# Kernel optimization log

Hardware: AMD Instinct MI355X
Metric: run time of the kernel (lower is better)

## Reference

```python
import jax, jax.numpy as jnp
import numpy as np

B, C, L, D, E, K = 64, 23, 26000, 64, 512, 3  # batch, chromosomes, bins/chr, d_model, eos_dim, num_states
V = C * L


def setup_inputs() -> dict:
    key = jax.random.key(0)
    k0, k1, k2, k3 = jax.random.split(key, 4)
    return {
        "eos_emb": jax.random.normal(k0, (B, C, E), jnp.float32),
        "bin_ids": jnp.arange(C * L, dtype=jnp.int32).reshape(C, L),
        "emb_table": jax.random.normal(k1, (V, D), jnp.float32) * 0.02,
        "eos_W": jax.random.normal(k2, (D, E), jnp.float32) / np.float32(np.sqrt(E)),
        "eos_b": jnp.zeros((D,), jnp.float32),
        "fc_W": jax.random.normal(k3, (K, 2 * D), jnp.float32) / np.float32(np.sqrt(2 * D)),
        "fc_b": jnp.zeros((K,), jnp.float32),
    }


def reference(eos_emb, bin_ids, emb_table, eos_W, eos_b, fc_W, fc_b):
    # eos_projection (use_eos_proj=True): [B,C,E] @ [D,E]^T + b -> [B,C,D]
    eos = jnp.einsum('bce,de->bcd', eos_emb, eos_W) + eos_b
    # per-chromosome embedding gather (bin_projection skipped: bin_emb_dim == d_model, use_bin_proj=False)
    bin_emb = emb_table[bin_ids]  # [C,L,D]
    # fc on concat([bin, eos]) == bin @ Wb^T + eos @ We^T + b (avoids materializing [B,C,L,2D])
    Wb, We = fc_W[:, :D], fc_W[:, D:]
    a = jnp.einsum('cld,kd->clk', bin_emb, Wb)          # [C,L,K]
    e = jnp.einsum('bcd,kd->bck', eos, We) + fc_b       # [B,C,K]
    return jax.nn.relu(a[None, :, :, :] + e[:, :, None, :])  # [B,C,L,K]
```

## Files before the change

kernel.cpp:

```cpp
#include <hip/hip_runtime.h>

#define NB 64
#define NC 23
#define NL 26000
#define ND 64
#define NE 512
#define NK 3
#define FP4   (NL * NK / 4)
#define CFP4  (NC * FP4)
#define CHUNK 438
#define NCHUNK 1024
#define GLSPAN 584

typedef float v4f __attribute__((ext_vector_type(4)));

__global__ __launch_bounds__(256) void eos_e_kernel(
    const float* __restrict__ eos_emb,
    const float* __restrict__ eos_W,
    const float* __restrict__ eos_b,
    const float* __restrict__ fc_W,
    const float* __restrict__ fc_b,
    float* __restrict__ e_out)
{
    const int bc = blockIdx.x;
    const int t  = threadIdx.x;
    const int q  = t & 3;
    const int d  = t >> 2;

    __shared__ v4f xs4[NE / 4];
    if (t < NE / 4)
        xs4[t] = reinterpret_cast<const v4f*>(eos_emb + (size_t)bc * NE)[t];
    __syncthreads();

    const v4f* wrow = reinterpret_cast<const v4f*>(eos_W + (size_t)d * NE);
    v4f acc = (v4f)(0.f);
    #pragma unroll 8
    for (int j = 0; j < NE / 16; ++j) {
        const int idx = q + 4 * j;
        acc += wrow[idx] * xs4[idx];
    }
    float p = (acc.x + acc.y) + (acc.z + acc.w);
    p += __shfl_xor(p, 1, 64);
    p += __shfl_xor(p, 2, 64);
    const float eosd = p + eos_b[d];

    __shared__ float part[4][NK];
    #pragma unroll
    for (int k = 0; k < NK; ++k) {
        float pk = eosd * fc_W[k * (2 * ND) + ND + d];
        pk += __shfl_xor(pk,  4, 64);
        pk += __shfl_xor(pk,  8, 64);
        pk += __shfl_xor(pk, 16, 64);
        pk += __shfl_xor(pk, 32, 64);
        if ((t & 63) == 0) part[t >> 6][k] = pk;
    }
    __syncthreads();
    if (t < NK)
        e_out[(size_t)bc * NK + t] =
            part[0][t] + part[1][t] + part[2][t] + part[3][t] + fc_b[t];
}

__global__ __launch_bounds__(256) void fused_kernel(
    const int*   __restrict__ bin_ids,
    const float* __restrict__ emb_table,
    const float* __restrict__ fc_W,
    const float* __restrict__ e_in,
    float* __restrict__ out)
{
    const int bx    = blockIdx.x;
    const int t     = threadIdx.x;
    const int base  = bx * CHUNK;
    const int gl_lo = bx * GLSPAN;

    __shared__ v4f   wb4[NK][ND / 4];
    __shared__ v4f   e4[3][NB][2];
    __shared__ float a_lds[GLSPAN * 3];

    const int c_lo = base / FP4;
    const int c_hi_raw = (base + CHUNK - 1) / FP4;
    const int c_hi = (c_hi_raw < NC) ? c_hi_raw : (NC - 1);

    if (t < NK * (ND / 4)) {
        const int k = t / (ND / 4), i = t % (ND / 4);
        wb4[k][i] = reinterpret_cast<const v4f*>(fc_W + (size_t)k * (2 * ND))[i];
    }
    {
        const int i = t;
        for (int it = i; it < 3 * NB * 2; it += 256) {
            const int p   = it / (NB * 2);
            const int rem = it - p * (NB * 2);
            const int bl  = rem >> 1;
            const int ci  = rem & 1;
            const int c   = ci ? c_hi : c_lo;
            const float* ep = e_in + ((size_t)bl * NC + c) * NK;
            const float e0 = ep[0], e1 = ep[1], e2 = ep[2];
            v4f v;
            if      (p == 0) { v.x = e0; v.y = e1; v.z = e2; v.w = e0; }
            else if (p == 1) { v.x = e1; v.y = e2; v.z = e0; v.w = e1; }
            else             { v.x = e2; v.y = e0; v.z = e1; v.w = e2; }
            e4[p][bl][ci] = v;
        }
    }
    __syncthreads();

    const int q = t & 3;
    const int r = t >> 2;
    #pragma unroll
    for (int pass = 0; pass < 10; ++pass) {
        const int rl = pass * 64 + r;
        const int gl = gl_lo + rl;
        if (rl < GLSPAN && gl < NC * NL) {
            const int row = bin_ids[gl];
            const v4f* er = reinterpret_cast<const v4f*>(emb_table + (size_t)row * ND);
            v4f s0 = (v4f)(0.f), s1 = (v4f)(0.f), s2 = (v4f)(0.f);
            #pragma unroll
            for (int j = 0; j < 4; ++j) {
                const int idx = q + 4 * j;
                const v4f v = er[idx];
                s0 += v * wb4[0][idx];
                s1 += v * wb4[1][idx];
                s2 += v * wb4[2][idx];
            }
            float a0 = (s0.x + s0.y) + (s0.z + s0.w);
            float a1 = (s1.x + s1.y) + (s1.z + s1.w);
            float a2 = (s2.x + s2.y) + (s2.z + s2.w);
            a0 += __shfl_xor(a0, 1, 64); a0 += __shfl_xor(a0, 2, 64);
            a1 += __shfl_xor(a1, 1, 64); a1 += __shfl_xor(a1, 2, 64);
            a2 += __shfl_xor(a2, 1, 64); a2 += __shfl_xor(a2, 2, 64);
            if (q < NK) {
                const float val = (q == 0) ? a0 : (q == 1) ? a1 : a2;
                a_lds[rl * 3 + q] = val;
            }
        }
    }
    __syncthreads();

    const int f0 = base + t;
    const int p0 = f0 % 3;
    const int ci0 = ((f0 / FP4) == c_lo) ? 0 : 1;
    const bool v0 = (f0 < CFP4);
    v4f a0v = (v4f)(0.f);
    if (v0) a0v = *reinterpret_cast<const v4f*>(&a_lds[t * 4]);

    const int t1 = 256 + t;
    const bool has1 = (t1 < CHUNK);
    const int f1 = base + t1;
    const int p1 = has1 ? (f1 % 3) : 0;
    const int ci1 = (has1 && (f1 / FP4) == c_lo) ? 0 : 1;
    const bool v1 = has1 && (f1 < CFP4);
    v4f a1v = (v4f)(0.f);
    if (v1) a1v = *reinterpret_cast<const v4f*>(&a_lds[t1 * 4]);

    v4f* o4 = reinterpret_cast<v4f*>(out);
    #pragma unroll 4
    for (int bl = 0; bl < NB; ++bl) {
        const size_t ob = (size_t)bl * CFP4;
        if (v0) {
            const v4f ev = e4[p0][bl][ci0];
            v4f o;
            o.x = fmaxf(a0v.x + ev.x, 0.f);
            o.y = fmaxf(a0v.y + ev.y, 0.f);
            o.z = fmaxf(a0v.z + ev.z, 0.f);
            o.w = fmaxf(a0v.w + ev.w, 0.f);
            __builtin_nontemporal_store(o, &o4[ob + f0]);
        }
        if (v1) {
            const v4f ev = e4[p1][bl][ci1];
            v4f o;
            o.x = fmaxf(a1v.x + ev.x, 0.f);
            o.y = fmaxf(a1v.y + ev.y, 0.f);
            o.z = fmaxf(a1v.z + ev.z, 0.f);
            o.w = fmaxf(a1v.w + ev.w, 0.f);
            __builtin_nontemporal_store(o, &o4[ob + f1]);
        }
    }
}

__global__ __launch_bounds__(256) void decoder_fused_kernel(
    const int*   __restrict__ bin_ids,
    const float* __restrict__ emb_table,
    const float* __restrict__ fc_W,
    const float* __restrict__ e_in,
    float* __restrict__ out)
{
    const int c   = blockIdx.y;
    const int tid = threadIdx.x;
    const int l   = blockIdx.x * 256 + tid;

    __shared__ float wb[NK][ND];
    __shared__ float es[NB * NK];

    if (tid < NK * ND)
        wb[tid / ND][tid % ND] = fc_W[(tid / ND) * (2 * ND) + (tid % ND)];
    if (tid < NB * NK) {
        int b = tid / NK, k = tid % NK;
        es[tid] = e_in[((size_t)b * NC + c) * NK + k];
    }
    __syncthreads();
    if (l >= NL) return;

    const int row = bin_ids[(size_t)c * NL + l];
    const float4* er = reinterpret_cast<const float4*>(emb_table + (size_t)row * ND);
    const float4* w0 = reinterpret_cast<const float4*>(wb[0]);
    const float4* w1 = reinterpret_cast<const float4*>(wb[1]);
    const float4* w2 = reinterpret_cast<const float4*>(wb[2]);

    float a0 = 0.f, a1 = 0.f, a2 = 0.f;
    #pragma unroll
    for (int i = 0; i < ND / 4; ++i) {
        float4 v  = er[i];
        float4 p0 = w0[i], p1 = w1[i], p2 = w2[i];
        a0 += v.x * p0.x + v.y * p0.y + v.z * p0.z + v.w * p0.w;
        a1 += v.x * p1.x + v.y * p1.y + v.z * p1.z + v.w * p1.w;
        a2 += v.x * p2.x + v.y * p2.y + v.z * p2.z + v.w * p2.w;
    }

    size_t obase = ((size_t)c * NL + l) * NK;
    const size_t bstride = (size_t)NC * NL * NK;
    #pragma unroll 4
    for (int b = 0; b < NB; ++b) {
        const float e0 = es[b * NK + 0];
        const float e1 = es[b * NK + 1];
        const float e2 = es[b * NK + 2];
        out[obase + 0] = fmaxf(a0 + e0, 0.f);
        out[obase + 1] = fmaxf(a1 + e1, 0.f);
        out[obase + 2] = fmaxf(a2 + e2, 0.f);
        obase += bstride;
    }
}

extern "C" void kernel_launch(void* const* d_in, const int* in_sizes, int n_in,
                              void* d_out, int out_size, void* d_ws, size_t ws_size,
                              hipStream_t stream) {
    const float* eos_emb   = (const float*)d_in[0];
    const int*   bin_ids   = (const int*)  d_in[1];
    const float* emb_table = (const float*)d_in[2];
    const float* eos_W     = (const float*)d_in[3];
    const float* eos_b     = (const float*)d_in[4];
    const float* fc_W      = (const float*)d_in[5];
    const float* fc_b      = (const float*)d_in[6];
    float*       out       = (float*)d_out;

    float* e_ws = (float*)d_ws;

    eos_e_kernel<<<NB * NC, 256, 0, stream>>>(eos_emb, eos_W, eos_b, fc_W, fc_b, e_ws);

    if (ws_size >= (size_t)NB * NC * NK * sizeof(float)) {
        fused_kernel<<<NCHUNK, 256, 0, stream>>>(bin_ids, emb_table, fc_W, e_ws, out);
    } else {
        dim3 grid((NL + 255) / 256, NC);
        decoder_fused_kernel<<<grid, 256, 0, stream>>>(bin_ids, emb_table, fc_W, e_ws, out);
    }
}
```

Baseline: 153.3 us.

## Merge eos projection and decoder into one cooperative kernel with grid sync

```diff
diff --git a/kernel.cpp b/kernel.cpp
--- a/kernel.cpp
+++ b/kernel.cpp
@@ -1,4 +1,6 @@
 #include <hip/hip_runtime.h>
+#include <hip/hip_cooperative_groups.h>
+namespace cg = cooperative_groups;
 
 #define NB 64
 #define NC 23
@@ -8,102 +10,93 @@
 #define NK 3
 #define FP4   (NL * NK / 4)
 #define CFP4  (NC * FP4)
+#define NBLK  1024
 #define CHUNK 438
-#define NCHUNK 1024
 #define GLSPAN 584
+#define NBC (NB * NC)
 
 typedef float v4f __attribute__((ext_vector_type(4)));
 
-__global__ __launch_bounds__(256) void eos_e_kernel(
+__global__ __launch_bounds__(256, 4) void coop_kernel(
     const float* __restrict__ eos_emb,
+    const int*   __restrict__ bin_ids,
+    const float* __restrict__ emb_table,
     const float* __restrict__ eos_W,
     const float* __restrict__ eos_b,
     const float* __restrict__ fc_W,
     const float* __restrict__ fc_b,
-    float* __restrict__ e_out)
+    float* __restrict__ e_ws,
+    float* __restrict__ out)
 {
-    const int bc = blockIdx.x;
+    const int bx = blockIdx.x;
     const int t  = threadIdx.x;
     const int q  = t & 3;
     const int d  = t >> 2;
 
-    __shared__ v4f xs4[NE / 4];
-    if (t < NE / 4)
-        xs4[t] = reinterpret_cast<const v4f*>(eos_emb + (size_t)bc * NE)[t];
-    __syncthreads();
-
-    const v4f* wrow = reinterpret_cast<const v4f*>(eos_W + (size_t)d * NE);
-    v4f acc = (v4f)(0.f);
-    #pragma unroll 8
-    for (int j = 0; j < NE / 16; ++j) {
-        const int idx = q + 4 * j;
-        acc += wrow[idx] * xs4[idx];
-    }
-    float p = (acc.x + acc.y) + (acc.z + acc.w);
-    p += __shfl_xor(p, 1, 64);
-    p += __shfl_xor(p, 2, 64);
-    const float eosd = p + eos_b[d];
-
+    __shared__ v4f   xs4[NE / 4];
     __shared__ float part[4][NK];
-    #pragma unroll
-    for (int k = 0; k < NK; ++k) {
-        float pk = eosd * fc_W[k * (2 * ND) + ND + d];
-        pk += __shfl_xor(pk,  4, 64);
-        pk += __shfl_xor(pk,  8, 64);
-        pk += __shfl_xor(pk, 16, 64);
-        pk += __shfl_xor(pk, 32, 64);
-        if ((t & 63) == 0) part[t >> 6][k] = pk;
-    }
-    __syncthreads();
-    if (t < NK)
-        e_out[(size_t)bc * NK + t] =
-            part[0][t] + part[1][t] + part[2][t] + part[3][t] + fc_b[t];
-}
-
-__global__ __launch_bounds__(256) void fused_kernel(
-    const int*   __restrict__ bin_ids,
-    const float* __restrict__ emb_table,
-    const float* __restrict__ fc_W,
-    const float* __restrict__ e_in,
-    float* __restrict__ out)
-{
-    const int bx    = blockIdx.x;
-    const int t     = threadIdx.x;
-    const int base  = bx * CHUNK;
-    const int gl_lo = bx * GLSPAN;
-
     __shared__ v4f   wb4[NK][ND / 4];
     __shared__ v4f   e4[3][NB][2];
     __shared__ float a_lds[GLSPAN * 3];
 
-    const int c_lo = base / FP4;
-    const int c_hi_raw = (base + CHUNK - 1) / FP4;
-    const int c_hi = (c_hi_raw < NC) ? c_hi_raw : (NC - 1);
+    for (int bc = bx; bc < NBC; bc += NBLK) {
+        if (t < NE / 4)
+            xs4[t] = reinterpret_cast<const v4f*>(eos_emb + (size_t)bc * NE)[t];
+        __syncthreads();
+        const v4f* wrow = reinterpret_cast<const v4f*>(eos_W + (size_t)d * NE);
+        v4f acc = (v4f)(0.f);
+        #pragma unroll 8
+        for (int j = 0; j < NE / 16; ++j) {
+            const int idx = q + 4 * j;
+            acc += wrow[idx] * xs4[idx];
+        }
+        float p = (acc.x + acc.y) + (acc.z + acc.w);
+        p += __shfl_xor(p, 1, 64);
+        p += __shfl_xor(p, 2, 64);
+        const float eosd = p + eos_b[d];
+        #pragma unroll
+        for (int k = 0; k < NK; ++k) {
+            float pk = eosd * fc_W[k * (2 * ND) + ND + d];
+            pk += __shfl_xor(pk,  4, 64);
+            pk += __shfl_xor(pk,  8, 64);
+            pk += __shfl_xor(pk, 16, 64);
+            pk += __shfl_xor(pk, 32, 64);
+            if ((t & 63) == 0) part[t >> 6][k] = pk;
+        }
+        __syncthreads();
+        if (t < NK)
+            e_ws[(size_t)bc * NK + t] =
+                part[0][t] + part[1][t] + part[2][t] + part[3][t] + fc_b[t];
+        __syncthreads();
+    }
+
+    cg::this_grid().sync();
+
+    const int base  = bx * CHUNK;
+    const int gl_lo = bx * GLSPAN;
+    const int c_lo  = base / FP4;
+    int c_hi = (base + CHUNK - 1) / FP4;
+    if (c_hi >= NC) c_hi = NC - 1;
 
     if (t < NK * (ND / 4)) {
         const int k = t / (ND / 4), i = t % (ND / 4);
         wb4[k][i] = reinterpret_cast<const v4f*>(fc_W + (size_t)k * (2 * ND))[i];
     }
-    {
-        const int i = t;
-        for (int it = i; it < 3 * NB * 2; it += 256) {
-            const int p   = it / (NB * 2);
-            const int rem = it - p * (NB * 2);
-            const int bl  = rem >> 1;
-            const int ci  = rem & 1;
-            const int c   = ci ? c_hi : c_lo;
-            const float* ep = e_in + ((size_t)bl * NC + c) * NK;
-            const float e0 = ep[0], e1 = ep[1], e2 = ep[2];
-            v4f v;
-            if      (p == 0) { v.x = e0; v.y = e1; v.z = e2; v.w = e0; }
-            else if (p == 1) { v.x = e1; v.y = e2; v.z = e0; v.w = e1; }
-            else             { v.x = e2; v.y = e0; v.z = e1; v.w = e2; }
-            e4[p][bl][ci] = v;
-        }
-    }
-    __syncthreads();
-
-    const int q = t & 3;
+    for (int it = t; it < 3 * NB * 2; it += 256) {
+        const int p   = it / (NB * 2);
+        const int rem = it - p * (NB * 2);
+        const int bl  = rem >> 1;
+        const int ci  = rem & 1;
+        const int c   = ci ? c_hi : c_lo;
+        const float* ep = e_ws + ((size_t)bl * NC + c) * NK;
+        const float e0 = ep[0], e1 = ep[1], e2 = ep[2];
+        v4f v;
+        if      (p == 0) { v.x = e0; v.y = e1; v.z = e2; v.w = e0; }
+        else if (p == 1) { v.x = e1; v.y = e2; v.z = e0; v.w = e1; }
+        else             { v.x = e2; v.y = e0; v.z = e1; v.w = e2; }
+        e4[p][bl][ci] = v;
+    }
+
     const int r = t >> 2;
     #pragma unroll
     for (int pass = 0; pass < 10; ++pass) {
@@ -135,26 +128,27 @@
     }
     __syncthreads();
 
-    const int f0 = base + t;
-    const int p0 = f0 % 3;
-    const int ci0 = ((f0 / FP4) == c_lo) ? 0 : 1;
+    const int c_split = (c_lo + 1) * FP4;
+    const int f0  = base + t;
+    const int p0  = f0 % 3;
+    const int ci0 = (f0 >= c_split) ? 1 : 0;
     const bool v0 = (f0 < CFP4);
     v4f a0v = (v4f)(0.f);
     if (v0) a0v = *reinterpret_cast<const v4f*>(&a_lds[t * 4]);
 
-    const int t1 = 256 + t;
+    const int t1  = 256 + t;
     const bool has1 = (t1 < CHUNK);
-    const int f1 = base + t1;
-    const int p1 = has1 ? (f1 % 3) : 0;
-    const int ci1 = (has1 && (f1 / FP4) == c_lo) ? 0 : 1;
+    const int f1  = base + t1;
+    const int p1  = has1 ? (f1 % 3) : 0;
+    const int ci1 = (has1 && f1 >= c_split) ? 1 : 0;
     const bool v1 = has1 && (f1 < CFP4);
     v4f a1v = (v4f)(0.f);
     if (v1) a1v = *reinterpret_cast<const v4f*>(&a_lds[t1 * 4]);
 
     v4f* o4 = reinterpret_cast<v4f*>(out);
+    size_t ob = 0;
     #pragma unroll 4
     for (int bl = 0; bl < NB; ++bl) {
-        const size_t ob = (size_t)bl * CFP4;
         if (v0) {
             const v4f ev = e4[p0][bl][ci0];
             v4f o;
@@ -162,7 +156,7 @@
             o.y = fmaxf(a0v.y + ev.y, 0.f);
             o.z = fmaxf(a0v.z + ev.z, 0.f);
             o.w = fmaxf(a0v.w + ev.w, 0.f);
-            __builtin_nontemporal_store(o, &o4[ob + f0]);
+            o4[ob + f0] = o;
         }
         if (v1) {
             const v4f ev = e4[p1][bl][ci1];
@@ -171,61 +165,160 @@
             o.y = fmaxf(a1v.y + ev.y, 0.f);
             o.z = fmaxf(a1v.z + ev.z, 0.f);
             o.w = fmaxf(a1v.w + ev.w, 0.f);
-            __builtin_nontemporal_store(o, &o4[ob + f1]);
-        }
-    }
-}
-
-__global__ __launch_bounds__(256) void decoder_fused_kernel(
-    const int*   __restrict__ bin_ids,
-    const float* __restrict__ emb_table,
-    const float* __restrict__ fc_W,
-    const float* __restrict__ e_in,
+            o4[ob + f1] = o;
+        }
+        ob += CFP4;
+    }
+}
+
+#define R7CHUNK 3504
+#define R7NCHUNK 128
+#define R7NJ 14
+#define R7GB 8
+
+__global__ __launch_bounds__(256) void eos_e_kernel(
+    const float* __restrict__ eos_emb, const float* __restrict__ eos_W,
+    const float* __restrict__ eos_b, const float* __restrict__ fc_W,
+    const float* __restrict__ fc_b, float* __restrict__ e_out)
+{
+    const int bc = blockIdx.x;
+    const int t  = threadIdx.x;
+    const int q  = t & 3;
+    const int d  = t >> 2;
+
+    __shared__ v4f xs4[NE / 4];
+    if (t < NE / 4)
+        xs4[t] = reinterpret_cast<const v4f*>(eos_emb + (size_t)bc * NE)[t];
+    __syncthreads();
+
+    const v4f* wrow = reinterpret_cast<const v4f*>(eos_W + (size_t)d * NE);
+    v4f acc = (v4f)(0.f);
+    #pragma unroll 8
+    for (int j = 0; j < NE / 16; ++j) {
+        const int idx = q + 4 * j;
+        acc += wrow[idx] * xs4[idx];
+    }
+    float p = (acc.x + acc.y) + (acc.z + acc.w);
+    p += __shfl_xor(p, 1, 64);
+    p += __shfl_xor(p, 2, 64);
+    const float eosd = p + eos_b[d];
+
+    __shared__ float part[4][NK];
+    #pragma unroll
+    for (int k = 0; k < NK; ++k) {
+        float pk = eosd * fc_W[k * (2 * ND) + ND + d];
+        pk += __shfl_xor(pk,  4, 64);
+        pk += __shfl_xor(pk,  8, 64);
+        pk += __shfl_xor(pk, 16, 64);
+        pk += __shfl_xor(pk, 32, 64);
+        if ((t & 63) == 0) part[t >> 6][k] = pk;
+    }
+    __syncthreads();
+    if (t < NK)
+        e_out[(size_t)bc * NK + t] =
+            part[0][t] + part[1][t] + part[2][t] + part[3][t] + fc_b[t];
+}
+
+__global__ __launch_bounds__(256) void a_kernel(
+    const int* __restrict__ bin_ids, const float* __restrict__ emb_table,
+    const float* __restrict__ fc_W, float* __restrict__ a_out)
+{
+    const int c = blockIdx.y;
+    const int t = threadIdx.x;
+    const int q = t & 3;
+    const int r = t >> 2;
+    const int l = blockIdx.x * 64 + r;
+
+    __shared__ v4f wb4[NK][ND / 4];
+    if (t < NK * (ND / 4)) {
+        const int k = t / (ND / 4), i = t % (ND / 4);
+        wb4[k][i] = reinterpret_cast<const v4f*>(fc_W + (size_t)k * (2 * ND))[i];
+    }
+    __syncthreads();
+    if (l >= NL) return;
+
+    const int row = bin_ids[(size_t)c * NL + l];
+    const v4f* er = reinterpret_cast<const v4f*>(emb_table + (size_t)row * ND);
+
+    v4f s0 = (v4f)(0.f), s1 = (v4f)(0.f), s2 = (v4f)(0.f);
+    #pragma unroll
+    for (int j = 0; j < 4; ++j) {
+        const int idx = q + 4 * j;
+        const v4f v = er[idx];
+        s0 += v * wb4[0][idx];
+        s1 += v * wb4[1][idx];
+        s2 += v * wb4[2][idx];
+    }
+    float a0 = (s0.x + s0.y) + (s0.z + s0.w);
+    float a1 = (s1.x + s1.y) + (s1.z + s1.w);
+    float a2 = (s2.x + s2.y) + (s2.z + s2.w);
+    a0 += __shfl_xor(a0, 1, 64); a0 += __shfl_xor(a0, 2, 64);
+    a1 += __shfl_xor(a1, 1, 64); a1 += __shfl_xor(a1, 2, 64);
+    a2 += __shfl_xor(a2, 1, 64); a2 += __shfl_xor(a2, 2, 64);
+
+    if (q < NK) {
+        const float val = (q == 0) ? a0 : (q == 1) ? a1 : a2;
+        a_out[((size_t)c * NL + l) * NK + q] = val;
+    }
+}
+
+__global__ __launch_bounds__(256) void bstream_kernel(
+    const float* __restrict__ a_in, const float* __restrict__ e_in,
     float* __restrict__ out)
 {
-    const int c   = blockIdx.y;
-    const int tid = threadIdx.x;
-    const int l   = blockIdx.x * 256 + tid;
-
-    __shared__ float wb[NK][ND];
-    __shared__ float es[NB * NK];
-
-    if (tid < NK * ND)
-        wb[tid / ND][tid % ND] = fc_W[(tid / ND) * (2 * ND) + (tid % ND)];
-    if (tid < NB * NK) {
-        int b = tid / NK, k = tid % NK;
-        es[tid] = e_in[((size_t)b * NC + c) * NK + k];
-    }
-    __syncthreads();
-    if (l >= NL) return;
-
-    const int row = bin_ids[(size_t)c * NL + l];
-    const float4* er = reinterpret_cast<const float4*>(emb_table + (size_t)row * ND);
-    const float4* w0 = reinterpret_cast<const float4*>(wb[0]);
-    const float4* w1 = reinterpret_cast<const float4*>(wb[1]);
-    const float4* w2 = reinterpret_cast<const float4*>(wb[2]);
-
-    float a0 = 0.f, a1 = 0.f, a2 = 0.f;
+    const int bx = blockIdx.x;
+    const int b0 = blockIdx.y * R7GB;
+    const int t  = threadIdx.x;
+
+    __shared__ v4f e4[3][NC][R7GB];
+    for (int i = t; i < 3 * NC * R7GB; i += 256) {
+        const int p   = i / (NC * R7GB);
+        const int rem = i - p * (NC * R7GB);
+        const int c   = rem / R7GB;
+        const int bl  = rem - c * R7GB;
+        const float* ep = e_in + ((size_t)(b0 + bl) * NC + c) * NK;
+        const float e0 = ep[0], e1 = ep[1], e2 = ep[2];
+        v4f v;
+        if      (p == 0) { v.x = e0; v.y = e1; v.z = e2; v.w = e0; }
+        else if (p == 1) { v.x = e1; v.y = e2; v.z = e0; v.w = e1; }
+        else             { v.x = e2; v.y = e0; v.z = e1; v.w = e2; }
+        e4[p][c][bl] = v;
+    }
+    __syncthreads();
+
+    const int base = bx * R7CHUNK;
+    const v4f* a4 = reinterpret_cast<const v4f*>(a_in);
+
+    v4f        av[R7NJ];
+    const v4f* eptr[R7NJ];
+    bool       gj[R7NJ];
     #pragma unroll
-    for (int i = 0; i < ND / 4; ++i) {
-        float4 v  = er[i];
-        float4 p0 = w0[i], p1 = w1[i], p2 = w2[i];
-        a0 += v.x * p0.x + v.y * p0.y + v.z * p0.z + v.w * p0.w;
-        a1 += v.x * p1.x + v.y * p1.y + v.z * p1.z + v.w * p1.w;
-        a2 += v.x * p2.x + v.y * p2.y + v.z * p2.z + v.w * p2.w;
-    }
-
-    size_t obase = ((size_t)c * NL + l) * NK;
-    const size_t bstride = (size_t)NC * NL * NK;
-    #pragma unroll 4
-    for (int b = 0; b < NB; ++b) {
-        const float e0 = es[b * NK + 0];
-        const float e1 = es[b * NK + 1];
-        const float e2 = es[b * NK + 2];
-        out[obase + 0] = fmaxf(a0 + e0, 0.f);
-        out[obase + 1] = fmaxf(a1 + e1, 0.f);
-        out[obase + 2] = fmaxf(a2 + e2, 0.f);
-        obase += bstride;
+    for (int j = 0; j < R7NJ; ++j) {
+        const int fo = j * 256 + t;
+        const int f  = base + fo;
+        gj[j] = (fo < R7CHUNK) && (f < CFP4);
+        const int fc = gj[j] ? f : 0;
+        eptr[j] = &e4[fc % 3][fc / FP4][0];
+        av[j]   = gj[j] ? a4[fc] : (v4f)(0.f);
+    }
+
+    v4f* o4 = reinterpret_cast<v4f*>(out);
+    size_t obase = (size_t)b0 * CFP4 + base;
+    #pragma unroll 2
+    for (int bl = 0; bl < R7GB; ++bl) {
+        #pragma unroll
+        for (int j = 0; j < R7NJ; ++j) {
+            if (gj[j]) {
+                const v4f ev = eptr[j][bl];
+                v4f o;
+                o.x = fmaxf(av[j].x + ev.x, 0.f);
+                o.y = fmaxf(av[j].y + ev.y, 0.f);
+                o.z = fmaxf(av[j].z + ev.z, 0.f);
+                o.w = fmaxf(av[j].w + ev.w, 0.f);
+                o4[obase + j * 256 + t] = o;
+            }
+        }
+        obase += CFP4;
     }
 }
 
@@ -241,14 +334,27 @@
     const float* fc_b      = (const float*)d_in[6];
     float*       out       = (float*)d_out;
 
-    float* e_ws = (float*)d_ws;
-
-    eos_e_kernel<<<NB * NC, 256, 0, stream>>>(eos_emb, eos_W, eos_b, fc_W, fc_b, e_ws);
-
-    if (ws_size >= (size_t)NB * NC * NK * sizeof(float)) {
-        fused_kernel<<<NCHUNK, 256, 0, stream>>>(bin_ids, emb_table, fc_W, e_ws, out);
-    } else {
-        dim3 grid((NL + 255) / 256, NC);
-        decoder_fused_kernel<<<grid, 256, 0, stream>>>(bin_ids, emb_table, fc_W, e_ws, out);
-    }
-}
+    float*  e_ws = (float*)d_ws;
+    const size_t a_off_bytes = 32768;
+    float*  a_ws = (float*)((char*)d_ws + a_off_bytes);
+    const size_t a_bytes = (size_t)NC * NL * NK * sizeof(float);
+
+    bool coop_ok = false;
+    if (ws_size >= a_off_bytes) {
+        void* args[] = {(void*)&eos_emb, (void*)&bin_ids, (void*)&emb_table,
+                        (void*)&eos_W, (void*)&eos_b, (void*)&fc_W, (void*)&fc_b,
+                        (void*)&e_ws, (void*)&out};
+        hipError_t err = hipLaunchCooperativeKernel((const void*)coop_kernel,
+                                                    dim3(NBLK), dim3(256),
+                                                    args, 0, stream);
+        coop_ok = (err == hipSuccess);
+    }
+
+    if (!coop_ok && ws_size >= a_off_bytes + a_bytes) {
+        eos_e_kernel<<<NB * NC, 256, 0, stream>>>(eos_emb, eos_W, eos_b, fc_W, fc_b, e_ws);
+        dim3 grid_a((NL + 63) / 64, NC);
+        a_kernel<<<grid_a, 256, 0, stream>>>(bin_ids, emb_table, fc_W, a_ws);
+        dim3 grid_b(R7NCHUNK, NB / R7GB);
+        bstream_kernel<<<grid_b, 256, 0, stream>>>(a_ws, e_ws, out);
+    }
+}
```

New measurement: 282.1 us. 1.84x slower.
